# Optimization experiments

Hardware: AMD Instinct MI355X
Metric: run time of the kernel (lower is better)

## Reference

```python
import jax, jax.numpy as jnp
import numpy as np

V, D, H, HD, L, F, T, B = 1024, 768, 12, 64, 8, 3072, 1024, 2
STD = 0.02
EPS = 1e-5


def setup_inputs() -> dict:
    key = jax.random.key(0)
    ks = jax.random.split(key, 8)
    n = jax.random.normal
    return {
        "input_ids": jax.random.randint(ks[0], (B, T), 0, V),
        "tok_emb": n(ks[1], (V, D), dtype=jnp.float32) * STD,   # tied with lm_head
        "pos_emb": n(ks[2], (1, T, D), dtype=jnp.float32) * STD,
        "ln1_w": jnp.ones((L, D)), "ln1_b": jnp.zeros((L, D)),
        "qkv_w": n(ks[3], (L, D, 3 * D), dtype=jnp.float32) * STD,
        "out_w": n(ks[4], (L, D, D), dtype=jnp.float32) * STD,
        "ln2_w": jnp.ones((L, D)), "ln2_b": jnp.zeros((L, D)),
        "ffn_w1": n(ks[5], (L, D, F), dtype=jnp.float32) * STD,
        "ffn_b1": jnp.zeros((L, F)),
        "ffn_w2": n(ks[6], (L, F, D), dtype=jnp.float32) * STD,
        "ffn_b2": jnp.zeros((L, D)),
        "lnf_w": jnp.ones((D,)), "lnf_b": jnp.zeros((D,)),
    }


def _layernorm(x, w, b):
    mu = x.mean(-1, keepdims=True)
    var = ((x - mu) ** 2).mean(-1, keepdims=True)
    return (x - mu) * jax.lax.rsqrt(var + EPS) * w + b


def _forward(input_ids, tok_emb, pos_emb, ln1_w, ln1_b, qkv_w, out_w,
             ln2_w, ln2_b, ffn_w1, ffn_b1, ffn_w2, ffn_b2, lnf_w, lnf_b):
    x = tok_emb[input_ids] + pos_emb[:, :T, :]          # (B, T, D)
    causal = jnp.tril(jnp.ones((T, T), dtype=bool))     # (T, T)
    neg_inf = jnp.finfo(x.dtype).min

    def block(x, p):
        l1w, l1b, qkvw, ow, l2w, l2b, w1, b1, w2, b2 = p
        h = _layernorm(x, l1w, l1b)
        qkv = h @ qkvw                                   # (B, T, 3D)
        q, k, v = jnp.split(qkv, 3, axis=-1)
        q = q.reshape(B, T, H, HD).transpose(0, 2, 1, 3)  # (B, H, T, HD)
        k = k.reshape(B, T, H, HD).transpose(0, 2, 1, 3)
        v = v.reshape(B, T, H, HD).transpose(0, 2, 1, 3)
        att = jnp.einsum('bhqd,bhkd->bhqk', q, k) * (1.0 / np.sqrt(HD))
        att = jnp.where(causal, att, neg_inf)
        att = jax.nn.softmax(att, axis=-1)
        y = jnp.einsum('bhqk,bhkd->bhqd', att, v)        # (B, H, T, HD)
        y = y.transpose(0, 2, 1, 3).reshape(B, T, D)
        x = x + y @ ow
        h = _layernorm(x, l2w, l2b)
        x = x + jax.nn.gelu(h @ w1 + b1, approximate=False) @ w2 + b2
        return x, None

    params = (ln1_w, ln1_b, qkv_w, out_w, ln2_w, ln2_b,
              ffn_w1, ffn_b1, ffn_w2, ffn_b2)
    x, _ = jax.lax.scan(block, x, params)
    x = _layernorm(x, lnf_w, lnf_b)
    return x @ tok_emb.T                                 # tied lm_head -> (B, T, V)


def reference(input_ids, tok_emb, pos_emb, ln1_w, ln1_b, qkv_w, out_w,
              ln2_w, ln2_b, ffn_w1, ffn_b1, ffn_w2, ffn_b2, lnf_w, lnf_b):
    return _forward(input_ids, tok_emb, pos_emb, ln1_w, ln1_b, qkv_w, out_w,
                    ln2_w, ln2_b, ffn_w1, ffn_b1, ffn_w2, ffn_b2, lnf_w, lnf_b)
```

## Files before the change

kernel.cpp:

```cpp
#include <hip/hip_runtime.h>
#include <hip/hip_bf16.h>
#include <math.h>

#define D_  768
#define T_  1024
#define B_  2
#define H_  12
#define HD_ 64
#define L_  8
#define F_  3072
#define V_  1024
#define M_  (B_ * T_)

typedef __bf16 bf16_t;
typedef __bf16 bf16x8 __attribute__((ext_vector_type(8)));
typedef float  f32x4  __attribute__((ext_vector_type(4)));

__device__ __forceinline__ void ld_g2l16(const bf16_t* g, bf16_t* l)
{
    __builtin_amdgcn_global_load_lds(
        (const __attribute__((address_space(1))) void*)g,
        (__attribute__((address_space(3))) void*)l,
        16, 0, 0);
}

__global__ __launch_bounds__(256) void embed_kernel(
    const int* __restrict__ ids, const float* __restrict__ tok,
    const float* __restrict__ pos, float* __restrict__ x)
{
    const int row = blockIdx.x;
    const int t   = row & (T_ - 1);
    const int id  = ids[row];
    const int c   = threadIdx.x;
#pragma unroll
    for (int i = 0; i < 3; ++i) {
        const int d = c + i * 256;
        x[(size_t)row * D_ + d] = tok[(size_t)id * D_ + d] + pos[(size_t)t * D_ + d];
    }
}

__global__ __launch_bounds__(256) void wtrans_kernel(
    const float* __restrict__ in, bf16_t* __restrict__ out, int K, int N)
{
    __shared__ float tile[32][33];
    const int n0 = blockIdx.x * 32, k0 = blockIdx.y * 32;
    const int tx = threadIdx.x & 31, ty = threadIdx.x >> 5;
#pragma unroll
    for (int i = 0; i < 4; ++i)
        tile[ty + 8 * i][tx] = in[(size_t)(k0 + ty + 8 * i) * N + n0 + tx];
    __syncthreads();
#pragma unroll
    for (int i = 0; i < 4; ++i) {
        const int n = ty + 8 * i;
        out[(size_t)(n0 + n) * K + k0 + tx] = (bf16_t)tile[tx][n];
    }
}

__global__ __launch_bounds__(256) void conv_kernel(
    const float* __restrict__ in, bf16_t* __restrict__ out)
{
    const int i = blockIdx.x * 1024 + threadIdx.x * 4;
    const f32x4 v = *(const f32x4*)(in + i);
#pragma unroll
    for (int j = 0; j < 4; ++j) out[i + j] = (bf16_t)v[j];
}

__device__ __forceinline__ float block_sum(float v)
{
    __shared__ float sm[4];
#pragma unroll
    for (int off = 32; off; off >>= 1) v += __shfl_down(v, off);
    if ((threadIdx.x & 63) == 0) sm[threadIdx.x >> 6] = v;
    __syncthreads();
    const float r = sm[0] + sm[1] + sm[2] + sm[3];
    __syncthreads();
    return r;
}

__global__ __launch_bounds__(256) void ln_kernel(
    const float* __restrict__ x, const float* __restrict__ w,
    const float* __restrict__ b, bf16_t* __restrict__ out)
{
    const int row = blockIdx.x;
    const float* xr = x + (size_t)row * D_;
    const int t = threadIdx.x;
    const float v0 = xr[t];
    const float v1 = xr[t + 256];
    const float v2 = xr[t + 512];
    const float mu = block_sum(v0 + v1 + v2) * (1.f / D_);
    const float d0 = v0 - mu, d1 = v1 - mu, d2 = v2 - mu;
    const float var = block_sum(d0 * d0 + d1 * d1 + d2 * d2) * (1.f / D_);
    const float rstd = rsqrtf(var + 1e-5f);
    bf16_t* o = out + (size_t)row * D_;
    o[t]       = (bf16_t)(d0 * rstd * w[t]       + b[t]);
    o[t + 256] = (bf16_t)(d1 * rstd * w[t + 256] + b[t + 256]);
    o[t + 512] = (bf16_t)(d2 * rstd * w[t + 512] + b[t + 512]);
}

template<int BN, bool RES, bool BIAS, bool GELU_, bool OUTF32>
__global__ __launch_bounds__(256) void gemm_bt(
    const bf16_t* __restrict__ A, const bf16_t* __restrict__ Bt,
    const float* __restrict__ bias, const float* __restrict__ res,
    void* __restrict__ Cp, int M, int N, int K)
{
    constexpr int BM = 64, BK = 64;
    constexpr int WN = BN / 2, NT = WN / 16;
    constexpr int AR = (BM * BK) / (256 * 8);
    constexpr int BR = (BN * BK) / (256 * 8);
    __shared__ bf16_t As[BM * BK];
    __shared__ bf16_t Bs[BN * BK];

    const int t    = threadIdx.x;
    const int wave = t >> 6, lane = t & 63;
    const int lr   = lane & 15, quad = lane >> 4;
    const int bm0  = blockIdx.y * BM, bn0 = blockIdx.x * BN;
    const int wm   = wave >> 1, wn = wave & 1;

    f32x4 acc[2][NT];
#pragma unroll
    for (int i = 0; i < 2; ++i)
#pragma unroll
        for (int j = 0; j < NT; ++j) { f32x4 z = {0.f, 0.f, 0.f, 0.f}; acc[i][j] = z; }

    const bf16_t* asrc[AR];
    const bf16_t* bsrc[BR];
#pragma unroll
    for (int rnd = 0; rnd < AR; ++rnd) {
        const int p = rnd * 256 + t, row = p >> 3, c = (p & 7) ^ (row & 7);
        asrc[rnd] = A + (size_t)(bm0 + row) * K + c * 8;
    }
#pragma unroll
    for (int rnd = 0; rnd < BR; ++rnd) {
        const int p = rnd * 256 + t, row = p >> 3, c = (p & 7) ^ (row & 7);
        bsrc[rnd] = Bt + (size_t)(bn0 + row) * K + c * 8;
    }

    for (int k0 = 0; k0 < K; k0 += BK) {
        __syncthreads();
#pragma unroll
        for (int rnd = 0; rnd < AR; ++rnd)
            ld_g2l16(asrc[rnd] + k0, As + (rnd * 256 + wave * 64) * 8);
#pragma unroll
        for (int rnd = 0; rnd < BR; ++rnd)
            ld_g2l16(bsrc[rnd] + k0, Bs + (rnd * 256 + wave * 64) * 8);
        __syncthreads();

#pragma unroll
        for (int ks = 0; ks < 2; ++ks) {
            const int ch = ((quad + 4 * ks) ^ (lr & 7)) * 8;
            const bf16x8 a0 = *(const bf16x8*)(As + (wm * 32 + lr) * BK + ch);
            const bf16x8 a1 = *(const bf16x8*)(As + (wm * 32 + 16 + lr) * BK + ch);
#pragma unroll
            for (int nt = 0; nt < NT; ++nt) {
                const bf16x8 b = *(const bf16x8*)(Bs + (wn * WN + nt * 16 + lr) * BK + ch);
                acc[0][nt] = __builtin_amdgcn_mfma_f32_16x16x32_bf16(a0, b, acc[0][nt], 0, 0, 0);
                acc[1][nt] = __builtin_amdgcn_mfma_f32_16x16x32_bf16(a1, b, acc[1][nt], 0, 0, 0);
            }
        }
    }

#pragma unroll
    for (int mt = 0; mt < 2; ++mt) {
        const int mbase = bm0 + wm * 32 + mt * 16 + quad * 4;
#pragma unroll
        for (int nt = 0; nt < NT; ++nt) {
            const int n = bn0 + wn * WN + nt * 16 + lr;
            const float bv = BIAS ? bias[n] : 0.f;
#pragma unroll
            for (int r = 0; r < 4; ++r) {
                const int m = mbase + r;
                float v = acc[mt][nt][r] + bv;
                if (RES)   v += res[(size_t)m * N + n];
                if (GELU_) v = 0.5f * v * (1.f + erff(v * 0.70710678118654752f));
                if (OUTF32) ((float*)Cp)[(size_t)m * N + n] = v;
                else        ((bf16_t*)Cp)[(size_t)m * N + n] = (bf16_t)v;
            }
        }
    }
}

__global__ __launch_bounds__(256) void attn_kernel(
    const bf16_t* __restrict__ qkv, bf16_t* __restrict__ y)
{
    __shared__ bf16_t Ks[64][72];
    __shared__ bf16_t Vt[64][72];
    __shared__ bf16_t Ps[4][16][72];

    const int q0   = blockIdx.x * 64;
    const int bh   = blockIdx.y;
    const int b    = bh / H_;
    const int hh   = bh % H_;
    const int t    = threadIdx.x;
    const int wave = t >> 6;
    const int lane = t & 63;
    const int lr   = lane & 15;
    const int quad = lane >> 4;

    const size_t qg = ((size_t)b * T_ + q0 + wave * 16 + lr) * (3 * D_) + hh * HD_;
    const bf16x8 aQ0 = *(const bf16x8*)(qkv + qg + quad * 8);
    const bf16x8 aQ1 = *(const bf16x8*)(qkv + qg + 32 + quad * 8);

    f32x4 o[4];
#pragma unroll
    for (int i = 0; i < 4; ++i) { f32x4 z = {0.f, 0.f, 0.f, 0.f}; o[i] = z; }
    float mrow[4] = {-1e30f, -1e30f, -1e30f, -1e30f};
    float lrow[4] = {0.f, 0.f, 0.f, 0.f};

    for (int kt = 0; kt <= (int)blockIdx.x; ++kt) {
        const int k_base = kt * 64;
        __syncthreads();

        {
            const int key = t >> 2, dc = (t & 3) * 8;
            const size_t g = ((size_t)b * T_ + k_base + key) * (3 * D_) + D_ + hh * HD_;
            *(bf16x8*)(&Ks[key][dc])      = *(const bf16x8*)(qkv + g + dc);
            *(bf16x8*)(&Ks[key][dc + 32]) = *(const bf16x8*)(qkv + g + dc + 32);
        }
        {
            const int key = lane;
            const size_t g = ((size_t)b * T_ + k_base + key) * (3 * D_) + 2 * D_ + hh * HD_ + wave * 16;
            const bf16x8 v0 = *(const bf16x8*)(qkv + g);
            const bf16x8 v1 = *(const bf16x8*)(qkv + g + 8);
#pragma unroll
            for (int i = 0; i < 8; ++i) {
                Vt[wave * 16 + i][key]     = v0[i];
                Vt[wave * 16 + 8 + i][key] = v1[i];
            }
        }
        __syncthreads();

        f32x4 s[4];
#pragma unroll
        for (int i = 0; i < 4; ++i) { f32x4 z = {0.f, 0.f, 0.f, 0.f}; s[i] = z; }
#pragma unroll
        for (int nt = 0; nt < 4; ++nt) {
            bf16x8 bk0 = *(const bf16x8*)(&Ks[nt * 16 + lr][quad * 8]);
            bf16x8 bk1 = *(const bf16x8*)(&Ks[nt * 16 + lr][32 + quad * 8]);
            s[nt] = __builtin_amdgcn_mfma_f32_16x16x32_bf16(aQ0, bk0, s[nt], 0, 0, 0);
            s[nt] = __builtin_amdgcn_mfma_f32_16x16x32_bf16(aQ1, bk1, s[nt], 0, 0, 0);
        }

#pragma unroll
        for (int r = 0; r < 4; ++r) {
            const int qg_i = q0 + wave * 16 + quad * 4 + r;
            float mx = -1e30f;
#pragma unroll
            for (int nt = 0; nt < 4; ++nt) {
                float sv = s[nt][r] * 0.125f;
                if (k_base + nt * 16 + lr > qg_i) sv = -1e30f;
                s[nt][r] = sv;
                mx = fmaxf(mx, sv);
            }
            mx = fmaxf(mx, __shfl_xor(mx, 1));
            mx = fmaxf(mx, __shfl_xor(mx, 2));
            mx = fmaxf(mx, __shfl_xor(mx, 4));
            mx = fmaxf(mx, __shfl_xor(mx, 8));
            const float mnew = fmaxf(mrow[r], mx);
            float ps = 0.f;
#pragma unroll
            for (int nt = 0; nt < 4; ++nt) {
                const float p = __expf(s[nt][r] - mnew);
                s[nt][r] = p;
                ps += p;
            }
            ps += __shfl_xor(ps, 1);
            ps += __shfl_xor(ps, 2);
            ps += __shfl_xor(ps, 4);
            ps += __shfl_xor(ps, 8);
            const float alpha = __expf(mrow[r] - mnew);
            lrow[r] = lrow[r] * alpha + ps;
            mrow[r] = mnew;
#pragma unroll
            for (int nt = 0; nt < 4; ++nt) o[nt][r] *= alpha;
        }

#pragma unroll
        for (int nt = 0; nt < 4; ++nt)
#pragma unroll
            for (int r = 0; r < 4; ++r)
                Ps[wave][quad * 4 + r][nt * 16 + lr] = (bf16_t)s[nt][r];

        const bf16x8 aP0 = *(const bf16x8*)(&Ps[wave][lr][quad * 8]);
        const bf16x8 aP1 = *(const bf16x8*)(&Ps[wave][lr][32 + quad * 8]);
#pragma unroll
        for (int nt = 0; nt < 4; ++nt) {
            bf16x8 bv0 = *(const bf16x8*)(&Vt[nt * 16 + lr][quad * 8]);
            bf16x8 bv1 = *(const bf16x8*)(&Vt[nt * 16 + lr][32 + quad * 8]);
            o[nt] = __builtin_amdgcn_mfma_f32_16x16x32_bf16(aP0, bv0, o[nt], 0, 0, 0);
            o[nt] = __builtin_amdgcn_mfma_f32_16x16x32_bf16(aP1, bv1, o[nt], 0, 0, 0);
        }
    }

#pragma unroll
    for (int r = 0; r < 4; ++r) {
        const float inv = 1.f / lrow[r];
        const size_t row = (size_t)b * T_ + q0 + wave * 16 + quad * 4 + r;
#pragma unroll
        for (int nt = 0; nt < 4; ++nt)
            y[row * D_ + hh * HD_ + nt * 16 + lr] = (bf16_t)(o[nt][r] * inv);
    }
}

extern "C" void kernel_launch(void* const* d_in, const int* in_sizes, int n_in,
                              void* d_out, int out_size, void* d_ws, size_t ws_size,
                              hipStream_t stream)
{
    const int*   ids  = (const int*)d_in[0];
    const float* tok  = (const float*)d_in[1];
    const float* pos  = (const float*)d_in[2];
    const float* l1w  = (const float*)d_in[3];
    const float* l1b  = (const float*)d_in[4];
    const float* qkvw = (const float*)d_in[5];
    const float* outw = (const float*)d_in[6];
    const float* l2w  = (const float*)d_in[7];
    const float* l2b  = (const float*)d_in[8];
    const float* w1   = (const float*)d_in[9];
    const float* b1   = (const float*)d_in[10];
    const float* w2   = (const float*)d_in[11];
    const float* b2   = (const float*)d_in[12];
    const float* lnfw = (const float*)d_in[13];
    const float* lnfb = (const float*)d_in[14];

    float*  x     = (float*)d_ws;
    bf16_t* h     = (bf16_t*)(x + (size_t)M_ * D_);
    bf16_t* qkv   = h     + (size_t)M_ * D_;
    bf16_t* y     = qkv   + (size_t)M_ * 3 * D_;
    bf16_t* mid   = y     + (size_t)M_ * D_;
    bf16_t* tokb  = mid   + (size_t)M_ * F_;
    bf16_t* wqkvT = tokb  + (size_t)V_ * D_;
    bf16_t* woutT = wqkvT + (size_t)3 * D_ * D_;
    bf16_t* w1T   = woutT + (size_t)D_ * D_;
    bf16_t* w2T   = w1T   + (size_t)F_ * D_;

    embed_kernel<<<M_, 256, 0, stream>>>(ids, tok, pos, x);
    conv_kernel<<<(V_ * D_) / 1024, 256, 0, stream>>>(tok, tokb);

    for (int l = 0; l < L_; ++l) {
        wtrans_kernel<<<dim3(3 * D_ / 32, D_ / 32), 256, 0, stream>>>(
            qkvw + (size_t)l * D_ * 3 * D_, wqkvT, D_, 3 * D_);
        wtrans_kernel<<<dim3(D_ / 32, D_ / 32), 256, 0, stream>>>(
            outw + (size_t)l * D_ * D_, woutT, D_, D_);
        wtrans_kernel<<<dim3(F_ / 32, D_ / 32), 256, 0, stream>>>(
            w1 + (size_t)l * D_ * F_, w1T, D_, F_);
        wtrans_kernel<<<dim3(D_ / 32, F_ / 32), 256, 0, stream>>>(
            w2 + (size_t)l * F_ * D_, w2T, F_, D_);

        ln_kernel<<<M_, 256, 0, stream>>>(x, l1w + l * D_, l1b + l * D_, h);
        gemm_bt<128, false, false, false, false><<<dim3(3 * D_ / 128, M_ / 64), 256, 0, stream>>>(
            h, wqkvT, nullptr, nullptr, qkv, M_, 3 * D_, D_);
        attn_kernel<<<dim3(T_ / 64, B_ * H_), 256, 0, stream>>>(qkv, y);
        gemm_bt<64, true, false, false, true><<<dim3(D_ / 64, M_ / 64), 256, 0, stream>>>(
            y, woutT, nullptr, x, x, M_, D_, D_);
        ln_kernel<<<M_, 256, 0, stream>>>(x, l2w + l * D_, l2b + l * D_, h);
        gemm_bt<128, false, true, true, false><<<dim3(F_ / 128, M_ / 64), 256, 0, stream>>>(
            h, w1T, b1 + (size_t)l * F_, nullptr, mid, M_, F_, D_);
        gemm_bt<64, true, true, false, true><<<dim3(D_ / 64, M_ / 64), 256, 0, stream>>>(
            mid, w2T, b2 + (size_t)l * D_, x, x, M_, D_, F_);
    }

    ln_kernel<<<M_, 256, 0, stream>>>(x, lnfw, lnfb, h);
    gemm_bt<64, false, false, false, true><<<dim3(V_ / 64, M_ / 64), 256, 0, stream>>>(
        h, tokb, nullptr, nullptr, d_out, M_, V_, D_);
}
```

Measured before the change: 1.363 ms.

## Batch weight transposes across layers and retile GEMM with BK=32 and larger blocks

All layers' weight transposes now run up front as batched launches using a z grid dimension, replacing four launches per layer, with per-layer offsets into enlarged transposed-weight buffers. The GEMM is rewritten with BK=32, a new 4-slot XOR swizzle, separate fragment loads per step, and configurable BM, giving 128x128 tiles for QKV and FFN1 and 64x128 for the others. This cuts launch count and raises per-block reuse, but needs more workspace for per-layer weights. It also halves the K step, which doubles the number of barriers per K loop, and the larger tiles mean fewer blocks.

Result: slower. 1.651 ms (+21.2%).

```diff
diff --git a/kernel.cpp b/kernel.cpp
--- a/kernel.cpp
+++ b/kernel.cpp
@@ -43,16 +43,18 @@
     const float* __restrict__ in, bf16_t* __restrict__ out, int K, int N)
 {
     __shared__ float tile[32][33];
+    const float* inl = in + (size_t)blockIdx.z * K * N;
+    bf16_t* outl = out + (size_t)blockIdx.z * N * K;
     const int n0 = blockIdx.x * 32, k0 = blockIdx.y * 32;
     const int tx = threadIdx.x & 31, ty = threadIdx.x >> 5;
 #pragma unroll
     for (int i = 0; i < 4; ++i)
-        tile[ty + 8 * i][tx] = in[(size_t)(k0 + ty + 8 * i) * N + n0 + tx];
+        tile[ty + 8 * i][tx] = inl[(size_t)(k0 + ty + 8 * i) * N + n0 + tx];
     __syncthreads();
 #pragma unroll
     for (int i = 0; i < 4; ++i) {
         const int n = ty + 8 * i;
-        out[(size_t)(n0 + n) * K + k0 + tx] = (bf16_t)tile[tx][n];
+        outl[(size_t)(n0 + n) * K + k0 + tx] = (bf16_t)tile[tx][n];
     }
 }
 
@@ -97,16 +99,15 @@
     o[t + 512] = (bf16_t)(d2 * rstd * w[t + 512] + b[t + 512]);
 }
 
-template<int BN, bool RES, bool BIAS, bool GELU_, bool OUTF32>
+template<int BM, int BN, bool RES, bool BIAS, bool GELU_, bool OUTF32>
 __global__ __launch_bounds__(256) void gemm_bt(
     const bf16_t* __restrict__ A, const bf16_t* __restrict__ Bt,
     const float* __restrict__ bias, const float* __restrict__ res,
     void* __restrict__ Cp, int M, int N, int K)
 {
-    constexpr int BM = 64, BK = 64;
-    constexpr int WN = BN / 2, NT = WN / 16;
-    constexpr int AR = (BM * BK) / (256 * 8);
-    constexpr int BR = (BN * BK) / (256 * 8);
+    constexpr int BK = 32;
+    constexpr int MT = BM / 32, NT = BN / 32;
+    constexpr int AR = BM / 64, BR = BN / 64;
     __shared__ bf16_t As[BM * BK];
     __shared__ bf16_t Bs[BN * BK];
 
@@ -116,9 +117,9 @@
     const int bm0  = blockIdx.y * BM, bn0 = blockIdx.x * BN;
     const int wm   = wave >> 1, wn = wave & 1;
 
-    f32x4 acc[2][NT];
-#pragma unroll
-    for (int i = 0; i < 2; ++i)
+    f32x4 acc[MT][NT];
+#pragma unroll
+    for (int i = 0; i < MT; ++i)
 #pragma unroll
         for (int j = 0; j < NT; ++j) { f32x4 z = {0.f, 0.f, 0.f, 0.f}; acc[i][j] = z; }
 
@@ -126,12 +127,14 @@
     const bf16_t* bsrc[BR];
 #pragma unroll
     for (int rnd = 0; rnd < AR; ++rnd) {
-        const int p = rnd * 256 + t, row = p >> 3, c = (p & 7) ^ (row & 7);
+        const int idx = rnd * 256 + t, row = idx >> 2, slot = idx & 3;
+        const int c = slot ^ ((row >> 1) & 3);
         asrc[rnd] = A + (size_t)(bm0 + row) * K + c * 8;
     }
 #pragma unroll
     for (int rnd = 0; rnd < BR; ++rnd) {
-        const int p = rnd * 256 + t, row = p >> 3, c = (p & 7) ^ (row & 7);
+        const int idx = rnd * 256 + t, row = idx >> 2, slot = idx & 3;
+        const int c = slot ^ ((row >> 1) & 3);
         bsrc[rnd] = Bt + (size_t)(bn0 + row) * K + c * 8;
     }
 
@@ -145,26 +148,32 @@
             ld_g2l16(bsrc[rnd] + k0, Bs + (rnd * 256 + wave * 64) * 8);
         __syncthreads();
 
-#pragma unroll
-        for (int ks = 0; ks < 2; ++ks) {
-            const int ch = ((quad + 4 * ks) ^ (lr & 7)) * 8;
-            const bf16x8 a0 = *(const bf16x8*)(As + (wm * 32 + lr) * BK + ch);
-            const bf16x8 a1 = *(const bf16x8*)(As + (wm * 32 + 16 + lr) * BK + ch);
-#pragma unroll
-            for (int nt = 0; nt < NT; ++nt) {
-                const bf16x8 b = *(const bf16x8*)(Bs + (wn * WN + nt * 16 + lr) * BK + ch);
-                acc[0][nt] = __builtin_amdgcn_mfma_f32_16x16x32_bf16(a0, b, acc[0][nt], 0, 0, 0);
-                acc[1][nt] = __builtin_amdgcn_mfma_f32_16x16x32_bf16(a1, b, acc[1][nt], 0, 0, 0);
-            }
-        }
-    }
-
-#pragma unroll
-    for (int mt = 0; mt < 2; ++mt) {
-        const int mbase = bm0 + wm * 32 + mt * 16 + quad * 4;
+        bf16x8 af[MT], bfr[NT];
+#pragma unroll
+        for (int mt = 0; mt < MT; ++mt) {
+            const int row = wm * (BM / 2) + mt * 16 + lr;
+            const int slot = quad ^ ((row >> 1) & 3);
+            af[mt] = *(const bf16x8*)(As + row * BK + slot * 8);
+        }
 #pragma unroll
         for (int nt = 0; nt < NT; ++nt) {
-            const int n = bn0 + wn * WN + nt * 16 + lr;
+            const int row = wn * (BN / 2) + nt * 16 + lr;
+            const int slot = quad ^ ((row >> 1) & 3);
+            bfr[nt] = *(const bf16x8*)(Bs + row * BK + slot * 8);
+        }
+#pragma unroll
+        for (int mt = 0; mt < MT; ++mt)
+#pragma unroll
+            for (int nt = 0; nt < NT; ++nt)
+                acc[mt][nt] = __builtin_amdgcn_mfma_f32_16x16x32_bf16(af[mt], bfr[nt], acc[mt][nt], 0, 0, 0);
+    }
+
+#pragma unroll
+    for (int mt = 0; mt < MT; ++mt) {
+        const int mbase = bm0 + wm * (BM / 2) + mt * 16 + quad * 4;
+#pragma unroll
+        for (int nt = 0; nt < NT; ++nt) {
+            const int n = bn0 + wn * (BN / 2) + nt * 16 + lr;
             const float bv = BIAS ? bias[n] : 0.f;
 #pragma unroll
             for (int r = 0; r < 4; ++r) {
@@ -328,37 +337,33 @@
     bf16_t* mid   = y     + (size_t)M_ * D_;
     bf16_t* tokb  = mid   + (size_t)M_ * F_;
     bf16_t* wqkvT = tokb  + (size_t)V_ * D_;
-    bf16_t* woutT = wqkvT + (size_t)3 * D_ * D_;
-    bf16_t* w1T   = woutT + (size_t)D_ * D_;
-    bf16_t* w2T   = w1T   + (size_t)F_ * D_;
+    bf16_t* woutT = wqkvT + (size_t)L_ * 3 * D_ * D_;
+    bf16_t* w1T   = woutT + (size_t)L_ * D_ * D_;
+    bf16_t* w2T   = w1T   + (size_t)L_ * F_ * D_;
 
     embed_kernel<<<M_, 256, 0, stream>>>(ids, tok, pos, x);
     conv_kernel<<<(V_ * D_) / 1024, 256, 0, stream>>>(tok, tokb);
 
+    wtrans_kernel<<<dim3(3 * D_ / 32, D_ / 32, L_), 256, 0, stream>>>(qkvw, wqkvT, D_, 3 * D_);
+    wtrans_kernel<<<dim3(D_ / 32, D_ / 32, L_),     256, 0, stream>>>(outw, woutT, D_, D_);
+    wtrans_kernel<<<dim3(F_ / 32, D_ / 32, L_),     256, 0, stream>>>(w1,   w1T,   D_, F_);
+    wtrans_kernel<<<dim3(D_ / 32, F_ / 32, L_),     256, 0, stream>>>(w2,   w2T,   F_, D_);
+
     for (int l = 0; l < L_; ++l) {
-        wtrans_kernel<<<dim3(3 * D_ / 32, D_ / 32), 256, 0, stream>>>(
-            qkvw + (size_t)l * D_ * 3 * D_, wqkvT, D_, 3 * D_);
-        wtrans_kernel<<<dim3(D_ / 32, D_ / 32), 256, 0, stream>>>(
-            outw + (size_t)l * D_ * D_, woutT, D_, D_);
-        wtrans_kernel<<<dim3(F_ / 32, D_ / 32), 256, 0, stream>>>(
-            w1 + (size_t)l * D_ * F_, w1T, D_, F_);
-        wtrans_kernel<<<dim3(D_ / 32, F_ / 32), 256, 0, stream>>>(
-            w2 + (size_t)l * F_ * D_, w2T, F_, D_);
-
         ln_kernel<<<M_, 256, 0, stream>>>(x, l1w + l * D_, l1b + l * D_, h);
-        gemm_bt<128, false, false, false, false><<<dim3(3 * D_ / 128, M_ / 64), 256, 0, stream>>>(
-            h, wqkvT, nullptr, nullptr, qkv, M_, 3 * D_, D_);
+        gemm_bt<128, 128, false, false, false, false><<<dim3(3 * D_ / 128, M_ / 128), 256, 0, stream>>>(
+            h, wqkvT + (size_t)l * 3 * D_ * D_, nullptr, nullptr, qkv, M_, 3 * D_, D_);
         attn_kernel<<<dim3(T_ / 64, B_ * H_), 256, 0, stream>>>(qkv, y);
-        gemm_bt<64, true, false, false, true><<<dim3(D_ / 64, M_ / 64), 256, 0, stream>>>(
-            y, woutT, nullptr, x, x, M_, D_, D_);
+        gemm_bt<64, 128, true, false, false, true><<<dim3(D_ / 128, M_ / 64), 256, 0, stream>>>(
+            y, woutT + (size_t)l * D_ * D_, nullptr, x, x, M_, D_, D_);
         ln_kernel<<<M_, 256, 0, stream>>>(x, l2w + l * D_, l2b + l * D_, h);
-        gemm_bt<128, false, true, true, false><<<dim3(F_ / 128, M_ / 64), 256, 0, stream>>>(
-            h, w1T, b1 + (size_t)l * F_, nullptr, mid, M_, F_, D_);
-        gemm_bt<64, true, true, false, true><<<dim3(D_ / 64, M_ / 64), 256, 0, stream>>>(
-            mid, w2T, b2 + (size_t)l * D_, x, x, M_, D_, F_);
+        gemm_bt<128, 128, false, true, true, false><<<dim3(F_ / 128, M_ / 128), 256, 0, stream>>>(
+            h, w1T + (size_t)l * F_ * D_, b1 + (size_t)l * F_, nullptr, mid, M_, F_, D_);
+        gemm_bt<64, 128, true, true, false, true><<<dim3(D_ / 128, M_ / 64), 256, 0, stream>>>(
+            mid, w2T + (size_t)l * D_ * F_, b2 + (size_t)l * D_, x, x, M_, D_, F_);
     }
 
     ln_kernel<<<M_, 256, 0, stream>>>(x, lnfw, lnfb, h);
-    gemm_bt<64, false, false, false, true><<<dim3(V_ / 64, M_ / 64), 256, 0, stream>>>(
+    gemm_bt<64, 128, false, false, false, true><<<dim3(V_ / 128, M_ / 64), 256, 0, stream>>>(
         h, tokb, nullptr, nullptr, d_out, M_, V_, D_);
 }
```
